# Kernel tuning notes

Hardware: AMD Instinct MI355X
Metric: run time of the kernel (lower is better)

Reference implementation:

```python
import jax, jax.numpy as jnp
import numpy as np


def setup_inputs() -> dict:
    key = jax.random.key(0)
    k1, k2, k3, k4 = jax.random.split(key, 4)
    b, c, h, w = 32, 512, 64, 64
    r = 16
    return {
        "x": jax.random.normal(k1, (b, c, h, w), dtype=jnp.float32),
        "mu": jax.random.uniform(k2, (b, 2), dtype=jnp.float32),
        "log_sigma_se": jnp.zeros((), dtype=jnp.float32),
        "w_fc1": jax.random.normal(k3, (c // r, c), dtype=jnp.float32) * 0.05,
        "w_fc2": jax.random.normal(k4, (c, c // r), dtype=jnp.float32) * 0.05,
    }


def reference(x, mu, log_sigma_se, w_fc1, w_fc2):
    b, c, h, w = x.shape
    sigma = jnp.exp(log_sigma_se)
    # grids in [0,1]; grid_x varies along h, grid_y along w ('ij' indexing)
    gx = jnp.linspace(0.0, 1.0, h)[:, None]          # (h,1)
    gy = jnp.linspace(0.0, 1.0, w)[None, :]          # (1,w)
    mu_h = mu[:, 0][:, None, None]                   # (b,1,1)
    mu_w = mu[:, 1][:, None, None]
    dx = gx[None, :, :] - mu_h                       # (b,h,w) via broadcast
    dy = gy[None, :, :] - mu_w
    kernel = jnp.exp(-(dx * dx + dy * dy) / (2.0 * sigma))   # (b,h,w)
    kernel = kernel / jnp.sum(kernel, axis=(1, 2), keepdims=True)
    squeezed = jnp.einsum('bchw,bhw->bc', x, kernel)          # (b,c)
    hid = jax.nn.relu(squeezed @ w_fc1.T)                     # (b,c//r)
    weights = jax.nn.sigmoid(hid @ w_fc2.T)                   # (b,c)
    return x * weights[:, :, None, None]
```

## Files before the change

kernel.cpp:

```cpp
#include <hip/hip_runtime.h>
#include <math.h>

#define BB 32
#define CC 512
#define HH 64
#define WW 64
#define RR 16
#define CR (CC / RR)

typedef float floatx4 __attribute__((ext_vector_type(4)));

__device__ __forceinline__ float wave_sum64(float v) {
    #pragma unroll
    for (int off = 32; off > 0; off >>= 1)
        v += __shfl_xor(v, off, 64);
    return v;
}

__global__ void k_squeeze(const float* __restrict__ x,
                          const float* __restrict__ mu,
                          const float* __restrict__ log_sigma,
                          float* __restrict__ sq) {
    __shared__ float s_kx[64];
    __shared__ float s_ky[64];
    int b = blockIdx.y;
    int tid = threadIdx.x;

    if (tid < 64) {
        float sigma = expf(log_sigma[0]);
        float inv2s = 1.0f / (2.0f * sigma);
        float g = (float)tid / 63.0f;
        float dh = g - mu[b * 2 + 0];
        float dw = g - mu[b * 2 + 1];
        float vx = expf(-dh * dh * inv2s);
        float vy = expf(-dw * dw * inv2s);
        float sx = wave_sum64(vx);
        float sy = wave_sum64(vy);
        s_kx[tid] = vx / sx;
        s_ky[tid] = vy / sy;
    }
    __syncthreads();

    int wv = tid >> 6;
    int lane = tid & 63;
    int c = blockIdx.x * 4 + wv;
    const floatx4* xp = (const floatx4*)(x + ((size_t)(b * CC + c)) * (HH * WW));
    int col = lane & 15;
    int hbase = lane >> 4;
    float a0 = 0.f, a1 = 0.f, a2 = 0.f, a3 = 0.f;
    #pragma unroll
    for (int it = 0; it < 16; ++it) {
        int h = hbase + it * 4;
        floatx4 v = xp[h * 16 + col];
        float kh = s_kx[h];
        a0 += v.x * kh; a1 += v.y * kh; a2 += v.z * kh; a3 += v.w * kh;
    }
    int w0 = col * 4;
    float partial = a0 * s_ky[w0] + a1 * s_ky[w0 + 1] + a2 * s_ky[w0 + 2] + a3 * s_ky[w0 + 3];
    float s = wave_sum64(partial);
    if (lane == 0) sq[b * CC + c] = s;
}

__global__ void k_mlp(const float* __restrict__ sq,
                      const float* __restrict__ w1,
                      const float* __restrict__ w2,
                      float* __restrict__ weights) {
    __shared__ float s_sq[CC];
    __shared__ float s_hid[CR];
    int b = blockIdx.x;
    int tid = threadIdx.x;
    for (int c = tid; c < CC; c += 256) s_sq[c] = sq[b * CC + c];
    __syncthreads();
    int j = tid >> 3;
    int seg = tid & 7;
    float acc = 0.f;
    const float* w1r = w1 + j * CC + seg * 64;
    const float* sqr = s_sq + seg * 64;
    #pragma unroll 8
    for (int c = 0; c < 64; ++c) acc += sqr[c] * w1r[c];
    acc += __shfl_xor(acc, 4, 64);
    acc += __shfl_xor(acc, 2, 64);
    acc += __shfl_xor(acc, 1, 64);
    if (seg == 0) s_hid[j] = fmaxf(acc, 0.0f);
    __syncthreads();
    for (int c = tid; c < CC; c += 256) {
        float a = 0.f;
        const float* w2r = w2 + c * CR;
        #pragma unroll
        for (int jj = 0; jj < CR; ++jj) a += s_hid[jj] * w2r[jj];
        weights[b * CC + c] = 1.0f / (1.0f + expf(-a));
    }
}

__global__ void k_scale(const float* __restrict__ x,
                        const float* __restrict__ wt,
                        float* __restrict__ out, long n4) {
    long gid = (long)blockIdx.x * blockDim.x + threadIdx.x;
    long stride = (long)gridDim.x * blockDim.x;
    long niter = n4 / stride;
    for (long j = niter; j-- > 0; ) {
        long i = j * stride + gid;
        floatx4 v = ((const floatx4*)x)[i];
        float s = wt[i >> 10];
        floatx4 o = v * s;
        __builtin_nontemporal_store(o, ((floatx4*)out) + i);
    }
}

extern "C" void kernel_launch(void* const* d_in, const int* in_sizes, int n_in,
                              void* d_out, int out_size, void* d_ws, size_t ws_size,
                              hipStream_t stream) {
    const float* x  = (const float*)d_in[0];
    const float* mu = (const float*)d_in[1];
    const float* ls = (const float*)d_in[2];
    const float* w1 = (const float*)d_in[3];
    const float* w2 = (const float*)d_in[4];
    float* out = (float*)d_out;

    float* ws = (float*)d_ws;
    float* sq = ws;
    float* wt = ws + 16384;

    k_squeeze<<<dim3(CC / 4, BB), 256, 0, stream>>>(x, mu, ls, sq);
    k_mlp<<<BB, 256, 0, stream>>>(sq, w1, w2, wt);
    k_scale<<<2048, 256, 0, stream>>>(x, wt, out, (long)BB * CC * HH * WW / 4);
}
```

Measured before the change: 133.5 us.

## Split batches into groups so scale pass rereads x from cache, fuse MLP

Launches squeeze and scale in two batch groups of 16, so the second pass over x for each group (about half the tensor) can be served from the last-level cache rather than HBM. The separate MLP kernel is removed. Each scale block now recomputes the fc1 hidden vector for its batch and computes sigmoid weights for its own 8 channels. This trades redundant small fc1 work per block, one extra kernel launch and the earlier reverse-order cache trick for a smaller working set per group.

```diff
diff --git a/kernel.cpp b/kernel.cpp
--- a/kernel.cpp
+++ b/kernel.cpp
@@ -7,6 +7,8 @@
 #define WW 64
 #define RR 16
 #define CR (CC / RR)
+#define BPG 16
+#define NGROUPS (BB / BPG)
 
 typedef float floatx4 __attribute__((ext_vector_type(4)));
 
@@ -20,10 +22,10 @@
 __global__ void k_squeeze(const float* __restrict__ x,
                           const float* __restrict__ mu,
                           const float* __restrict__ log_sigma,
-                          float* __restrict__ sq) {
+                          float* __restrict__ sq, int b0) {
     __shared__ float s_kx[64];
     __shared__ float s_ky[64];
-    int b = blockIdx.y;
+    int b = b0 + blockIdx.y;
     int tid = threadIdx.x;
 
     if (tid < 64) {
@@ -61,49 +63,53 @@
     if (lane == 0) sq[b * CC + c] = s;
 }
 
-__global__ void k_mlp(const float* __restrict__ sq,
-                      const float* __restrict__ w1,
-                      const float* __restrict__ w2,
-                      float* __restrict__ weights) {
+__global__ void k_scale_fused(const float* __restrict__ x,
+                              const float* __restrict__ sq,
+                              const float* __restrict__ w1,
+                              const float* __restrict__ w2,
+                              float* __restrict__ out, int b0) {
     __shared__ float s_sq[CC];
     __shared__ float s_hid[CR];
-    int b = blockIdx.x;
+    __shared__ float s_w[8];
+    int b = b0 + blockIdx.y;
+    int c0 = blockIdx.x * 8;
     int tid = threadIdx.x;
-    for (int c = tid; c < CC; c += 256) s_sq[c] = sq[b * CC + c];
+
+    for (int i = tid; i < CC; i += 256) s_sq[i] = sq[b * CC + i];
     __syncthreads();
-    int j = tid >> 3;
-    int seg = tid & 7;
-    float acc = 0.f;
-    const float* w1r = w1 + j * CC + seg * 64;
-    const float* sqr = s_sq + seg * 64;
-    #pragma unroll 8
-    for (int c = 0; c < 64; ++c) acc += sqr[c] * w1r[c];
-    acc += __shfl_xor(acc, 4, 64);
-    acc += __shfl_xor(acc, 2, 64);
-    acc += __shfl_xor(acc, 1, 64);
-    if (seg == 0) s_hid[j] = fmaxf(acc, 0.0f);
+
+    {
+        int j = tid >> 3;
+        int seg = tid & 7;
+        float acc = 0.f;
+        const float* w1r = w1 + j * CC + seg * 64;
+        const float* sqr = s_sq + seg * 64;
+        #pragma unroll 8
+        for (int c = 0; c < 64; ++c) acc += sqr[c] * w1r[c];
+        acc += __shfl_xor(acc, 4, 64);
+        acc += __shfl_xor(acc, 2, 64);
+        acc += __shfl_xor(acc, 1, 64);
+        if (seg == 0) s_hid[j] = fmaxf(acc, 0.0f);
+    }
     __syncthreads();
-    for (int c = tid; c < CC; c += 256) {
+
+    if (tid < 8) {
+        const float* w2r = w2 + (c0 + tid) * CR;
         float a = 0.f;
-        const float* w2r = w2 + c * CR;
         #pragma unroll
         for (int jj = 0; jj < CR; ++jj) a += s_hid[jj] * w2r[jj];
-        weights[b * CC + c] = 1.0f / (1.0f + expf(-a));
+        s_w[tid] = 1.0f / (1.0f + expf(-a));
     }
-}
+    __syncthreads();
 
-__global__ void k_scale(const float* __restrict__ x,
-                        const float* __restrict__ wt,
-                        float* __restrict__ out, long n4) {
-    long gid = (long)blockIdx.x * blockDim.x + threadIdx.x;
-    long stride = (long)gridDim.x * blockDim.x;
-    long niter = n4 / stride;
-    for (long j = niter; j-- > 0; ) {
-        long i = j * stride + gid;
-        floatx4 v = ((const floatx4*)x)[i];
-        float s = wt[i >> 10];
-        floatx4 o = v * s;
-        __builtin_nontemporal_store(o, ((floatx4*)out) + i);
+    const floatx4* xp = (const floatx4*)(x + ((size_t)(b * CC + c0)) * (HH * WW));
+    floatx4* op = (floatx4*)(out + ((size_t)(b * CC + c0)) * (HH * WW));
+    #pragma unroll 8
+    for (int it = 0; it < 32; ++it) {
+        int idx = it * 256 + tid;
+        float s = s_w[idx >> 10];
+        floatx4 v = xp[idx];
+        __builtin_nontemporal_store(v * s, op + idx);
     }
 }
 
@@ -117,11 +123,11 @@
     const float* w2 = (const float*)d_in[4];
     float* out = (float*)d_out;
 
-    float* ws = (float*)d_ws;
-    float* sq = ws;
-    float* wt = ws + 16384;
+    float* sq = (float*)d_ws;
 
-    k_squeeze<<<dim3(CC / 4, BB), 256, 0, stream>>>(x, mu, ls, sq);
-    k_mlp<<<BB, 256, 0, stream>>>(sq, w1, w2, wt);
-    k_scale<<<2048, 256, 0, stream>>>(x, wt, out, (long)BB * CC * HH * WW / 4);
+    for (int g = 0; g < NGROUPS; ++g) {
+        int b0 = g * BPG;
+        k_squeeze<<<dim3(CC / 4, BPG), 256, 0, stream>>>(x, mu, ls, sq, b0);
+        k_scale_fused<<<dim3(64, BPG), 256, 0, stream>>>(x, sq, w1, w2, out, b0);
+    }
 }
```

Result: slower. 145.8 us (+9.2%).
